# Kernel tuning notes

Hardware: AMD Instinct MI355X
Metric: run time of the kernel (lower is better)

## Reference

```python
import jax, jax.numpy as jnp
import numpy as np

ALPHA = 0.2          # LeakyReLU negative slope
NEG_INF = -9e15      # mask fill value used by the original module


def setup_inputs() -> dict:
    key = jax.random.key(0)
    k1, k2, k3, k4 = jax.random.split(key, 4)
    N, F_in, F_out = 8192, 256, 64
    h = jax.random.normal(k1, (N, F_in), dtype=jnp.float32)
    adj = jax.random.randint(k2, (N, N), 0, 2).astype(jnp.int32)
    # xavier_uniform with gain=1.414
    gain = 1.414
    bW = gain * np.sqrt(6.0 / (F_in + F_out))
    W = jax.random.uniform(k3, (F_in, F_out), dtype=jnp.float32, minval=-bW, maxval=bW)
    ba = gain * np.sqrt(6.0 / (2 * F_out + 1))
    a = jax.random.uniform(k4, (2 * F_out, 1), dtype=jnp.float32, minval=-ba, maxval=ba)
    return {"h": h, "adj": adj, "W": W, "a": a}


def reference(h, adj, W, a):
    # Wh: [N, F_out]
    Wh = h @ W
    F_out = Wh.shape[1]
    # Decompose a_input @ a: e[i, j] = leakyrelu(Wh[j]@a[:F] + Wh[i]@a[F:])
    # (repeat gives Wh[j] in the first half, repeat_interleave gives Wh[i] in the second)
    f_src = (Wh @ a[:F_out]).reshape(-1)   # [N], coefficient of column index j
    f_dst = (Wh @ a[F_out:]).reshape(-1)   # [N], coefficient of row index i
    e = jax.nn.leaky_relu(f_dst[:, None] + f_src[None, :], negative_slope=ALPHA)  # [N, N]
    attention = jnp.where(adj > 0, e, NEG_INF)
    attention = jax.nn.softmax(attention, axis=1)
    # dropout is identity in eval mode (training=False)
    h_prime = attention @ Wh               # [N, F_out]
    return jax.nn.elu(h_prime)             # concat=True path
```

## Files before the change

kernel.cpp:

```cpp
#include <hip/hip_runtime.h>
#include <hip/hip_bf16.h>

#define GN     8192
#define FIN    256
#define FOUT   64
#define NSPLIT 8
#define JSEG   1024
#define NCH    32
#define PF     4
#define ROWS_B 128
#define LOG2E  1.44269504f

typedef float  f32x4  __attribute__((ext_vector_type(4)));
typedef __bf16 bf16x8 __attribute__((ext_vector_type(8)));
typedef int    iv4    __attribute__((ext_vector_type(4)));

__device__ __forceinline__ unsigned short f2bf_rtne(float x) {
    unsigned int u = __float_as_uint(x);
    unsigned int r = (u + 0x7FFFu + ((u >> 16) & 1u)) >> 16;
    return (unsigned short)r;
}

__global__ __launch_bounds__(256) void k_wh(const float* __restrict__ h,
                                            const float* __restrict__ W,
                                            const float* __restrict__ a,
                                            float* __restrict__ fsrc,
                                            float* __restrict__ fdst,
                                            uint4* __restrict__ whfrag) {
    __shared__ float Wt[FOUT][FIN + 1];
    __shared__ float WhL[32][FOUT + 1];
    int t = threadIdx.x;
    int col = t & 63, kq4 = t >> 6;
#pragma unroll
    for (int rep = 0; rep < 16; ++rep) {
        int k0 = kq4 * 4 + rep * 16;
        float4 wv;
        wv.x = W[(k0 + 0) * FOUT + col];
        wv.y = W[(k0 + 1) * FOUT + col];
        wv.z = W[(k0 + 2) * FOUT + col];
        wv.w = W[(k0 + 3) * FOUT + col];
        *(float4*)&Wt[col][k0] = wv;
    }
    __syncthreads();
    int wave = t >> 6, lane = t & 63;
    float a1 = a[lane], a2 = a[FOUT + lane];
    int bid = blockIdx.x;
#pragma unroll
    for (int rr = 0; rr < 8; ++rr) {
        int il = wave * 8 + rr;
        int i  = bid * 32 + il;
        const float* hrow = h + (size_t)i * FIN;
        float acc = 0.f;
#pragma unroll 8
        for (int k0 = 0; k0 < FIN; k0 += 4) {
            float4 hv = *(const float4*)&hrow[k0];
            float4 wv = *(const float4*)&Wt[lane][k0];
            acc += hv.x * wv.x + hv.y * wv.y + hv.z * wv.z + hv.w * wv.w;
        }
        WhL[il][lane] = acc;
        float v1 = acc * a1, v2 = acc * a2;
#pragma unroll
        for (int off = 32; off > 0; off >>= 1) {
            v1 += __shfl_xor(v1, off);
            v2 += __shfl_xor(v2, off);
        }
        if (lane == 0) {
            fsrc[i] = fminf(v1, 30.f) * LOG2E;
            fdst[i] = fminf(v2, 30.f) * LOG2E;
        }
    }
    __syncthreads();
    int lane2 = t & 63, ct = t >> 6;
    int colc = ct * 16 + (lane2 & 15);
    int gb = lane2 >> 4;
    unsigned int pk[4];
#pragma unroll
    for (int p = 0; p < 4; ++p) {
        int jo = ((p >> 1) * 16) + gb * 4 + (p & 1) * 2;
        unsigned int lo = f2bf_rtne(WhL[jo    ][colc]);
        unsigned int hi = f2bf_rtne(WhL[jo + 1][colc]);
        pk[p] = lo | (hi << 16);
    }
    uint4 o; o.x = pk[0]; o.y = pk[1]; o.z = pk[2]; o.w = pk[3];
    whfrag[(size_t)(bid * 4 + ct) * 64 + lane2] = o;
}

__global__ __launch_bounds__(512, 2) void k_attn(const int* __restrict__ adj,
                                                 const float* __restrict__ fsrc,
                                                 const float* __restrict__ fdst,
                                                 const uint4* __restrict__ whfrag,
                                                 float* __restrict__ pacc,
                                                 float* __restrict__ pden) {
    __shared__ uint4 whL[NCH * 4 * 64];
    __shared__ float fsL[JSEG];

    int t = threadIdx.x, wv = t >> 6, lane = t & 63;
    int bid = blockIdx.x;
    int rt = bid >> 3, q = bid & (NSPLIT - 1);
    int rowbase = rt * ROWS_B;

    {
        const uint4* src = whfrag + (size_t)q * (NCH * 4 * 64);
#pragma unroll
        for (int it = 0; it < 16; ++it) whL[it * 512 + t] = src[it * 512 + t];
        if (t < 256) *(float4*)&fsL[t * 4] = *(const float4*)&fsrc[q * JSEG + t * 4];
    }
    __syncthreads();

    int r = lane & 15, g = lane >> 4;
    int row = rowbase + wv * 16 + r;
    float d = fdst[row];
    const int* arow = adj + (size_t)row * GN + q * JSEG + g * 4;

    f32x4 acc0 = {0.f, 0.f, 0.f, 0.f}, acc1 = acc0, acc2 = acc0, acc3 = acc0;
    float den = 0.f;

    iv4 pfa[PF], pfb[PF];
#pragma unroll
    for (int dd = 0; dd < PF; ++dd) {
        pfa[dd] = *(const iv4*)(arow + dd * 32);
        pfb[dd] = *(const iv4*)(arow + dd * 32 + 16);
    }

    for (int cb = 0; cb < NCH; cb += PF) {
#pragma unroll
        for (int dd = 0; dd < PF; ++dd) {
            int ch = cb + dd;
            int ae[8] = {pfa[dd][0], pfa[dd][1], pfa[dd][2], pfa[dd][3],
                         pfb[dd][0], pfb[dd][1], pfb[dd][2], pfb[dd][3]};
            float4 s0 = *(const float4*)&fsL[ch * 32 + g * 4];
            float4 s1 = *(const float4*)&fsL[ch * 32 + 16 + g * 4];
            float se[8] = {s0.x, s0.y, s0.z, s0.w, s1.x, s1.y, s1.z, s1.w};

            int nch = ch + PF;
            if (nch < NCH) {
                pfa[dd] = *(const iv4*)(arow + nch * 32);
                pfb[dd] = *(const iv4*)(arow + nch * 32 + 16);
            }

            bf16x8 af;
            float ws = 0.f;
#pragma unroll
            for (int e = 0; e < 8; ++e) {
                float ev = d + se[e];
                float lr = fmaxf(ev, 0.2f * ev);
                float ex = __builtin_amdgcn_exp2f(lr);
                float wvv = (ae[e] > 0) ? ex : 0.f;
                ws += wvv;
                af[e] = (__bf16)wvv;
            }
            den += ws;

            const uint4* bl = &whL[(ch * 4) * 64 + lane];
            uint4 b0 = bl[0], b1 = bl[64], b2 = bl[128], b3 = bl[192];
            acc0 = __builtin_amdgcn_mfma_f32_16x16x32_bf16(af, __builtin_bit_cast(bf16x8, b0), acc0, 0, 0, 0);
            acc1 = __builtin_amdgcn_mfma_f32_16x16x32_bf16(af, __builtin_bit_cast(bf16x8, b1), acc1, 0, 0, 0);
            acc2 = __builtin_amdgcn_mfma_f32_16x16x32_bf16(af, __builtin_bit_cast(bf16x8, b2), acc2, 0, 0, 0);
            acc3 = __builtin_amdgcn_mfma_f32_16x16x32_bf16(af, __builtin_bit_cast(bf16x8, b3), acc3, 0, 0, 0);
        }
    }

    den += __shfl_xor(den, 16);
    den += __shfl_xor(den, 32);

    float* po = pacc + (size_t)q * (GN * FOUT);
    int orow = rowbase + wv * 16 + g * 4;
#pragma unroll
    for (int reg = 0; reg < 4; ++reg) {
        po[(size_t)(orow + reg) * FOUT +  0 + r] = acc0[reg];
        po[(size_t)(orow + reg) * FOUT + 16 + r] = acc1[reg];
        po[(size_t)(orow + reg) * FOUT + 32 + r] = acc2[reg];
        po[(size_t)(orow + reg) * FOUT + 48 + r] = acc3[reg];
    }
    if (g == 0) pden[(size_t)q * GN + row] = den;
}

__global__ __launch_bounds__(256) void k_out(const float* __restrict__ pacc,
                                             const float* __restrict__ pden,
                                             float* __restrict__ out) {
    int idx = blockIdx.x * 256 + threadIdx.x;
    int i = idx >> 6;
    float num = 0.f, den = 0.f;
#pragma unroll
    for (int qq = 0; qq < NSPLIT; ++qq) {
        num += pacc[(size_t)qq * (GN * FOUT) + idx];
        den += pden[(size_t)qq * GN + i];
    }
    float v = (den != 0.f) ? num / den : 0.f;
    out[idx] = v > 0.f ? v : __expf(v) - 1.f;
}

extern "C" void kernel_launch(void* const* d_in, const int* in_sizes, int n_in,
                              void* d_out, int out_size, void* d_ws, size_t ws_size,
                              hipStream_t stream) {
    (void)in_sizes; (void)n_in; (void)out_size; (void)ws_size;
    const float* h   = (const float*)d_in[0];
    const int*   adj = (const int*)d_in[1];
    const float* W   = (const float*)d_in[2];
    const float* a   = (const float*)d_in[3];
    float* out = (float*)d_out;

    float* ws     = (float*)d_ws;
    float* fsrc   = ws;
    float* fdst   = fsrc + GN;
    uint4* whfrag = (uint4*)(fdst + GN);
    float* pacc   = (float*)(whfrag + (size_t)GN / 32 * 4 * 64);
    float* pden   = pacc + (size_t)NSPLIT * GN * FOUT;

    k_wh  <<<GN / 32,                    256, 0, stream>>>(h, W, a, fsrc, fdst, whfrag);
    k_attn<<<(GN / ROWS_B) * NSPLIT,     512, 0, stream>>>(adj, fsrc, fdst, whfrag, pacc, pden);
    k_out <<<GN * FOUT / 256,            256, 0, stream>>>(pacc, pden, out);
}
```

Baseline: 106.2 us.

## Load adjacency row-contiguously per wave and compress to bitmasks via ballot

Each wave now reads its 16 adjacency rows with fully coalesced 1KB-per-row loads (64 lanes x 16 bytes) instead of strided per-lane 16-byte pieces. The rows are converted with ballots into packed bitmasks stored in a small per-wave LDS buffer, and the bit matching each attention element is extracted in the MFMA loop. The next group's adjacency loads are issued before the compute on the current group. This aims to make HBM reads of the dominant 256MB adjacency stream more efficient, at the cost of 64 registers of staging, ballot and LDS overhead, and reduced occupancy.

```diff
diff --git a/kernel.cpp b/kernel.cpp
--- a/kernel.cpp
+++ b/kernel.cpp
@@ -7,7 +7,7 @@
 #define NSPLIT 8
 #define JSEG   1024
 #define NCH    32
-#define PF     4
+#define GRP    4
 #define ROWS_B 128
 #define LOG2E  1.44269504f
 
@@ -93,11 +93,20 @@
                                                  float* __restrict__ pden) {
     __shared__ uint4 whL[NCH * 4 * 64];
     __shared__ float fsL[JSEG];
+    __shared__ unsigned bbuf[8][2][16][4];
 
     int t = threadIdx.x, wv = t >> 6, lane = t & 63;
     int bid = blockIdx.x;
     int rt = bid >> 3, q = bid & (NSPLIT - 1);
     int rowbase = rt * ROWS_B;
+    int r = lane & 15, g = lane >> 4;
+    int row16 = rowbase + wv * 16;
+
+    const int* abase = adj + (size_t)row16 * GN + q * JSEG;
+    iv4 st[16];
+#pragma unroll
+    for (int k = 0; k < 16; ++k)
+        st[k] = *(const iv4*)(abase + (size_t)k * GN + lane * 4);
 
     {
         const uint4* src = whfrag + (size_t)q * (NCH * 4 * 64);
@@ -107,37 +116,41 @@
     }
     __syncthreads();
 
-    int r = lane & 15, g = lane >> 4;
-    int row = rowbase + wv * 16 + r;
-    float d = fdst[row];
-    const int* arow = adj + (size_t)row * GN + q * JSEG + g * 4;
-
+    float d = fdst[row16 + r];
     f32x4 acc0 = {0.f, 0.f, 0.f, 0.f}, acc1 = acc0, acc2 = acc0, acc3 = acc0;
     float den = 0.f;
 
-    iv4 pfa[PF], pfb[PF];
-#pragma unroll
-    for (int dd = 0; dd < PF; ++dd) {
-        pfa[dd] = *(const iv4*)(arow + dd * 32);
-        pfb[dd] = *(const iv4*)(arow + dd * 32 + 16);
-    }
-
-    for (int cb = 0; cb < NCH; cb += PF) {
-#pragma unroll
-        for (int dd = 0; dd < PF; ++dd) {
-            int ch = cb + dd;
-            int ae[8] = {pfa[dd][0], pfa[dd][1], pfa[dd][2], pfa[dd][3],
-                         pfb[dd][0], pfb[dd][1], pfb[dd][2], pfb[dd][3]};
+    for (int grp = 0; grp < GRP; ++grp) {
+#pragma unroll
+        for (int k = 0; k < 16; ++k) {
+            iv4 v = st[k];
+            unsigned long long b0 = __ballot(v[0] > 0);
+            unsigned long long b1 = __ballot(v[1] > 0);
+            unsigned long long b2 = __ballot(v[2] > 0);
+            unsigned long long b3 = __ballot(v[3] > 0);
+            if (lane < 8) {
+                unsigned long long s01 = (lane & 1) ? b1 : b0;
+                unsigned long long s23 = (lane & 1) ? b3 : b2;
+                unsigned long long ss  = (lane & 2) ? s23 : s01;
+                bbuf[wv][lane >> 2][k][lane & 3] = (unsigned)(ss >> ((lane >> 2) * 32));
+            }
+        }
+        if (grp + 1 < GRP) {
+#pragma unroll
+            for (int k = 0; k < 16; ++k)
+                st[k] = *(const iv4*)(abase + (size_t)k * GN + (grp + 1) * 256 + lane * 4);
+        }
+#pragma unroll 4
+        for (int chl = 0; chl < 8; ++chl) {
+            int ch = grp * 8 + chl;
+            uint4 W4 = *(const uint4*)&bbuf[wv][chl >> 2][r][0];
             float4 s0 = *(const float4*)&fsL[ch * 32 + g * 4];
             float4 s1 = *(const float4*)&fsL[ch * 32 + 16 + g * 4];
+            const uint4* bl = &whL[(ch * 4) * 64 + lane];
+            uint4 b0 = bl[0], b1 = bl[64], b2 = bl[128], b3 = bl[192];
+            unsigned wc[4] = {W4.x, W4.y, W4.z, W4.w};
             float se[8] = {s0.x, s0.y, s0.z, s0.w, s1.x, s1.y, s1.z, s1.w};
-
-            int nch = ch + PF;
-            if (nch < NCH) {
-                pfa[dd] = *(const iv4*)(arow + nch * 32);
-                pfb[dd] = *(const iv4*)(arow + nch * 32 + 16);
-            }
-
+            int sb = (chl & 3) * 8 + g;
             bf16x8 af;
             float ws = 0.f;
 #pragma unroll
@@ -145,14 +158,12 @@
                 float ev = d + se[e];
                 float lr = fmaxf(ev, 0.2f * ev);
                 float ex = __builtin_amdgcn_exp2f(lr);
-                float wvv = (ae[e] > 0) ? ex : 0.f;
+                unsigned bit = (wc[e & 3] >> (sb + (e >> 2) * 4)) & 1u;
+                float wvv = bit ? ex : 0.f;
                 ws += wvv;
                 af[e] = (__bf16)wvv;
             }
             den += ws;
-
-            const uint4* bl = &whL[(ch * 4) * 64 + lane];
-            uint4 b0 = bl[0], b1 = bl[64], b2 = bl[128], b3 = bl[192];
             acc0 = __builtin_amdgcn_mfma_f32_16x16x32_bf16(af, __builtin_bit_cast(bf16x8, b0), acc0, 0, 0, 0);
             acc1 = __builtin_amdgcn_mfma_f32_16x16x32_bf16(af, __builtin_bit_cast(bf16x8, b1), acc1, 0, 0, 0);
             acc2 = __builtin_amdgcn_mfma_f32_16x16x32_bf16(af, __builtin_bit_cast(bf16x8, b2), acc2, 0, 0, 0);
@@ -172,7 +183,7 @@
         po[(size_t)(orow + reg) * FOUT + 32 + r] = acc2[reg];
         po[(size_t)(orow + reg) * FOUT + 48 + r] = acc3[reg];
     }
-    if (g == 0) pden[(size_t)q * GN + row] = den;
+    if (g == 0) pden[(size_t)q * GN + row16 + r] = den;
 }
 
 __global__ __launch_bounds__(256) void k_out(const float* __restrict__ pacc,
@@ -207,7 +218,7 @@
     float* pacc   = (float*)(whfrag + (size_t)GN / 32 * 4 * 64);
     float* pden   = pacc + (size_t)NSPLIT * GN * FOUT;
 
-    k_wh  <<<GN / 32,                    256, 0, stream>>>(h, W, a, fsrc, fdst, whfrag);
-    k_attn<<<(GN / ROWS_B) * NSPLIT,     512, 0, stream>>>(adj, fsrc, fdst, whfrag, pacc, pden);
-    k_out <<<GN * FOUT / 256,            256, 0, stream>>>(pacc, pden, out);
-}
+    k_wh  <<<GN / 32,                 256, 0, stream>>>(h, W, a, fsrc, fdst, whfrag);
+    k_attn<<<(GN / ROWS_B) * NSPLIT,  512, 0, stream>>>(adj, fsrc, fdst, whfrag, pacc, pden);
+    k_out <<<GN * FOUT / 256,         256, 0, stream>>>(pacc, pden, out);
+}
```

Result: slower. 111.9 us (+5.3%).
